# Optimization experiments

Hardware: AMD Instinct MI355X
Metric: run time of the kernel (lower is better)

## Reference

```python
import jax, jax.numpy as jnp
import numpy as np

B, D, E, G, P, H = 8192, 2048, 8, 4, 512, 192
T, DT, TAU, VTH, VRESET = 20, 0.001, 0.02, 0.5, 0.0
DELTA0, KTOP, KROUTE, PREDW = 7.0, 32, 2, 0.1


def setup_inputs() -> dict:
    key = jax.random.key(0)
    ks = jax.random.split(key, 12)
    s = 0.02
    return {
        "query_embedding": jax.random.normal(ks[0], (B, D), jnp.float32),
        "Wg": jax.random.normal(ks[1], (2, E), jnp.float32) * s,
        "bg": jnp.zeros((E,), jnp.float32),
        "Wp": jax.random.normal(ks[2], (2, E), jnp.float32) * s,
        "bp": jnp.zeros((E,), jnp.float32),
        "Wgg": jax.random.normal(ks[3], (2, G), jnp.float32) * s,
        "bgg": jnp.zeros((G,), jnp.float32),
        "W1": jax.random.normal(ks[4], (E, D, P), jnp.float32) * (1.0 / np.sqrt(D)),
        "b1": jnp.zeros((E, P), jnp.float32),
        "W2": jax.random.normal(ks[5], (E, P, D), jnp.float32) * (1.0 / np.sqrt(P)),
        "b2": jnp.zeros((E, D), jnp.float32),
    }


def reference(query_embedding, Wg, bg, Wp, bp, Wgg, bgg, W1, b1, W2, b2):
    x = query_embedding  # [B, D], already embed_dim -> no pad/slice
    dtype = x.dtype

    # --- Phasor bank temporal features on per-row mean ---
    qm = jnp.mean(x, axis=-1)  # [B]
    freqs = DELTA0 * jnp.arange(1, H + 1, dtype=dtype)  # [H]
    ang = qm[:, None] * freqs[None, :]  # [B, H]
    temporal = jnp.concatenate([jnp.cos(ang), jnp.sin(ang)], axis=-1)  # [B, 2H]

    # --- Spiking attention over top-K |x| indices (LIF over T steps) ---
    topk_idx = jax.lax.top_k(jnp.abs(x), KTOP)[1]  # [B, K]
    rows = jnp.arange(B)[:, None]
    I = jnp.zeros((B, D), dtype).at[rows, topk_idx].add(1.0)  # input current [B, vocab=D]

    def lif_step(v, _):
        v = v * (1.0 - DT / TAU) + I
        spike = (v >= VTH).astype(dtype)
        v = jnp.where(spike > 0, VRESET, v)
        return v, spike

    _, spikes = jax.lax.scan(lif_step, jnp.zeros((B, D), dtype), None, length=T)
    attention_gains = jnp.mean(spikes, axis=0)  # [B, D] spike rates

    # --- Bio gating inputs ---
    gate_in = jnp.stack([jnp.mean(temporal, axis=-1), jnp.mean(attention_gains, axis=-1)], axis=-1)  # [B, 2]

    gate_logits = gate_in @ Wg + bg  # [B, E]
    gate_logits = gate_logits - PREDW * (gate_in @ Wp + bp)

    # group routing bias: experts grouped round-robin i % G
    group_logits = gate_in @ Wgg + bgg  # [B, G]
    gmap = jax.nn.one_hot(jnp.arange(E) % G, G, dtype=dtype)  # [E, G]
    gate_logits = gate_logits + group_logits @ gmap.T

    gate_weights = jax.nn.softmax(gate_logits, axis=-1)  # temperature = 1

    # top-k routing + renormalization
    _, tidx = jax.lax.top_k(gate_weights, KROUTE)
    mask = jnp.zeros_like(gate_weights).at[rows, tidx].set(1.0)
    gated = gate_weights * mask
    gate_weights = gated / (jnp.sum(gated, axis=-1, keepdims=True) + 1e-9)

    # --- Dense MLP experts (bottleneck P = hidden // 4) ---
    h = jax.nn.relu(jnp.einsum('bd,edp->ebp', x, W1) + b1[:, None, :])  # [E, B, P]
    expert_out = jnp.einsum('ebp,eph->ebh', h, W2) + b2[:, None, :]  # [E, B, D]

    # gate-weighted combine
    context = jnp.einsum('be,ebh->bh', gate_weights, expert_out)  # [B, D]
    return context
```

## Files before the change

kernel.cpp:

```cpp
#include <hip/hip_runtime.h>
#include <stdint.h>

#define NB 8192
#define ND 2048
#define NE 8
#define NG 4
#define NP 512
#define NH 192

typedef _Float16 half_t;
typedef half_t f16x8 __attribute__((ext_vector_type(8)));
typedef float f32x4 __attribute__((ext_vector_type(4)));

__device__ __forceinline__ void gload16(const void* g, void* l) {
  __builtin_amdgcn_global_load_lds(
      (const __attribute__((address_space(1))) void*)g,
      (__attribute__((address_space(3))) void*)l, 16, 0, 0);
}

__global__ __launch_bounds__(256) void k_convert(
    const float* __restrict__ x, half_t* __restrict__ xh, double* __restrict__ qm)
{
  const int b = blockIdx.x;
  const int t = threadIdx.x;
  const float* xr = x + (size_t)b * ND;
  const float4 v0 = ((const float4*)xr)[t * 2];
  const float4 v1 = ((const float4*)xr)[t * 2 + 1];
  float f[8] = {v0.x, v0.y, v0.z, v0.w, v1.x, v1.y, v1.z, v1.w};
  double s = 0.0;
  __align__(16) half_t hb[8];
#pragma unroll
  for (int i = 0; i < 8; i++) { s += (double)f[i]; hb[i] = (half_t)f[i]; }
  *reinterpret_cast<int4*>(xh + (size_t)b * ND + t * 8) = *reinterpret_cast<const int4*>(hb);

#pragma unroll
  for (int m = 32; m >= 1; m >>= 1) s += __shfl_xor(s, m);
  __shared__ double part[4];
  if ((t & 63) == 0) part[t >> 6] = s;
  __syncthreads();
  if (t == 0) qm[b] = (part[0] + part[1] + part[2] + part[3]) / (double)ND;
}

__global__ __launch_bounds__(256) void k_gate(
    const double* __restrict__ qm,
    const float* __restrict__ Wg, const float* __restrict__ bg,
    const float* __restrict__ Wp, const float* __restrict__ bp,
    const float* __restrict__ Wgg, const float* __restrict__ bgg,
    int* __restrict__ e0a, int* __restrict__ e1a,
    float* __restrict__ w0a, float* __restrict__ w1a)
{
  const int wave = threadIdx.x >> 6;
  const int lane = threadIdx.x & 63;
  const int b = blockIdx.x * 4 + wave;
  const double q = qm[b];

  double part = 0.0;
#pragma unroll
  for (int i = 0; i < 3; i++) {
    int h = lane + i * 64;
    double ang = q * (7.0 * (double)(h + 1));
    part += cos(ang) + sin(ang);
  }
#pragma unroll
  for (int m = 32; m >= 1; m >>= 1) part += __shfl_xor(part, m);
  const double tm = part / (2.0 * (double)NH);
  const double gi1 = 32.0 / 2048.0;

  double lg = -1.0e300;
  if (lane < 8) {
    const int e = lane, g = e & 3;
    lg = tm * (double)Wg[e] + gi1 * (double)Wg[NE + e] + (double)bg[e];
    lg -= 0.1 * (tm * (double)Wp[e] + gi1 * (double)Wp[NE + e] + (double)bp[e]);
    lg += tm * (double)Wgg[g] + gi1 * (double)Wgg[NG + g] + (double)bgg[g];
  }
  double mx = lg;
#pragma unroll
  for (int m = 4; m >= 1; m >>= 1) mx = fmax(mx, __shfl_xor(mx, m));
  double pe = 0.0;
  if (lane < 8) pe = exp(lg - mx);
  double ps = pe;
#pragma unroll
  for (int m = 4; m >= 1; m >>= 1) ps += __shfl_xor(ps, m);

  double lgs[8], pes[8];
#pragma unroll
  for (int e = 0; e < 8; e++) { lgs[e] = __shfl(lg, e); pes[e] = __shfl(pe, e); }

  if (lane == 0) {
    int e0 = 0;
    for (int e = 1; e < NE; e++) if (lgs[e] > lgs[e0]) e0 = e;
    int e1 = (e0 == 0) ? 1 : 0;
    for (int e = 0; e < NE; e++) if (e != e0 && lgs[e] > lgs[e1]) e1 = e;
    const double p0 = pes[e0] / ps;
    const double p1 = pes[e1] / ps;
    const double den = p0 + p1 + 1e-9;
    e0a[b] = e0; e1a[b] = e1;
    w0a[b] = (float)(p0 / den);
    w1a[b] = (float)(p1 / den);
  }
}

__global__ __launch_bounds__(256) void k_bucket(
    const int* __restrict__ e0a, const int* __restrict__ e1a,
    const float* __restrict__ w0a, const float* __restrict__ w1a,
    int* __restrict__ rowl, float* __restrict__ wl, int* __restrict__ cnt,
    int* __restrict__ pos0a, int* __restrict__ pos1a,
    int* __restrict__ rowlp, int* __restrict__ cntp)
{
  const int t = threadIdx.x;
  const int r = blockIdx.x * 256 + t;
  __shared__ int hist[16], base[16], cursor[16];
  __shared__ int histp[64], basep[64], cursorp[64];
  if (t < 16) { hist[t] = 0; cursor[t] = 0; }
  if (t < 64) { histp[t] = 0; cursorp[t] = 0; }
  __syncthreads();

  const int e0 = e0a[r], e1 = e1a[r];
  const int p = e0 * 8 + e1;
  atomicAdd(&hist[e0], 1);
  atomicAdd(&hist[8 + e1], 1);
  atomicAdd(&histp[p], 1);
  __syncthreads();
  if (t < 16) base[t] = atomicAdd(&cnt[t], hist[t]);
  if (t < 64) basep[t] = atomicAdd(&cntp[t], histp[t]);
  __syncthreads();

  int p0 = atomicAdd(&cursor[e0], 1);
  int idx0 = base[e0] + p0;
  rowl[e0 * NB + idx0] = r;
  wl[e0 * NB + idx0] = w0a[r];
  pos0a[r] = idx0;

  int p1 = atomicAdd(&cursor[8 + e1], 1);
  int idx1 = base[8 + e1] + p1;
  rowl[(8 + e1) * NB + idx1] = r;
  wl[(8 + e1) * NB + idx1] = w1a[r];
  pos1a[r] = idx1;

  int pp = atomicAdd(&cursorp[p], 1);
  rowlp[p * NB + basep[p] + pp] = r;
}

__global__ __launch_bounds__(256) void k_cvt_w(
    const float* __restrict__ W1, const float* __restrict__ W2,
    half_t* __restrict__ w1t, half_t* __restrict__ w2t)
{
  const int which = blockIdx.y;
  const int R = which ? NP : ND;
  const int C = which ? ND : NP;
  const float* src = which ? W2 : W1;
  half_t* dst = which ? w2t : w1t;
  const int tiles_c = C >> 5;
  const int tiles_per_e = (R >> 5) * tiles_c;
  int id = blockIdx.x;
  int e = id / tiles_per_e;
  int rem = id - e * tiles_per_e;
  int tr = rem / tiles_c, tc = rem - tr * tiles_c;
  __shared__ float tile[32][33];
  const int tx = threadIdx.x & 31, ty = threadIdx.x >> 5;
  const float* s = src + (size_t)e * R * C + (size_t)(tr * 32) * C + tc * 32;
#pragma unroll
  for (int i = 0; i < 4; i++)
    tile[ty + i * 8][tx] = s[(size_t)(ty + i * 8) * C + tx];
  __syncthreads();
  half_t* d = dst + (size_t)e * R * C + (size_t)(tc * 32) * R + tr * 32;
#pragma unroll
  for (int i = 0; i < 4; i++)
    d[(size_t)(ty + i * 8) * R + tx] = (half_t)tile[tx][ty + i * 8];
}

__global__ void k_prefix(const int* __restrict__ cnt, const int* __restrict__ cntp,
                         int* __restrict__ pbase,
                         int* __restrict__ i16b, int* __restrict__ i16m, int* __restrict__ n16,
                         int* __restrict__ ipp, int* __restrict__ ipm, int* __restrict__ np)
{
  if (threadIdx.x == 0 && blockIdx.x == 0) {
    int s = 0;
    for (int i = 0; i < 16; i++) { pbase[i] = s; s += cnt[i]; }
    int t = 0;
    for (int b = 0; b < 16; b++)
      for (int m0 = 0; m0 < cnt[b]; m0 += 128) { i16b[t] = b; i16m[t] = m0; t++; }
    *n16 = t;
    t = 0;
    for (int p = 0; p < 64; p++)
      for (int m0 = 0; m0 < cntp[p]; m0 += 128) { ipp[t] = p; ipm[t] = m0; t++; }
    *np = t;
  }
}

__global__ __launch_bounds__(256, 2) void k_gemm1(
    const half_t* __restrict__ xh, const half_t* __restrict__ w1t,
    const float* __restrict__ b1,
    const int* __restrict__ rowl, const float* __restrict__ wl,
    const int* __restrict__ cnt, const int* __restrict__ pbase,
    const int* __restrict__ i16b, const int* __restrict__ i16m,
    const int* __restrict__ n16, half_t* __restrict__ Hbuf)
{
  const int wi = blockIdx.y;
  if (wi >= *n16) return;
  const int bucket = i16b[wi];
  const int m0 = i16m[wi];
  const int count = cnt[bucket];
  const int e = bucket & 7;
  const int n0 = blockIdx.x * 256;
  const int t = threadIdx.x;

  __shared__ __align__(16) half_t As[3][128 * 32];
  __shared__ __align__(16) half_t Bs[3][256 * 32];
  __shared__ int rows_s[128];
  __shared__ float ws_s[128];

  if (t < 128) {
    int mi = m0 + t;
    int idx = bucket * NB + (mi < count ? mi : m0);
    rows_s[t] = rowl[idx];
    ws_s[t] = wl[idx];
  }
  __syncthreads();

  const int w = t >> 6, lane = t & 63;
  const int cA0 = (w * 2) * 64 + lane, cA1 = cA0 + 64;
  const int rA0 = cA0 >> 2, rA1 = cA1 >> 2;
  const int kA0 = ((cA0 & 3) ^ ((rA0 >> 1) & 3)) * 8;
  const int kA1 = ((cA1 & 3) ^ ((rA1 >> 1) & 3)) * 8;
  const half_t* gA0 = xh + (size_t)rows_s[rA0] * ND + kA0;
  const half_t* gA1 = xh + (size_t)rows_s[rA1] * ND + kA1;
  const half_t* w1te = w1t + (size_t)e * NP * ND;
  const int cB0 = (w * 4) * 64 + lane, cB1 = cB0 + 64, cB2 = cB0 + 128, cB3 = cB0 + 192;
  const int rB0 = cB0 >> 2, rB1 = cB1 >> 2, rB2 = cB2 >> 2, rB3 = cB3 >> 2;
  const half_t* gB0 = w1te + (size_t)(n0 + rB0) * ND + ((cB0 & 3) ^ ((rB0 >> 1) & 3)) * 8;
  const half_t* gB1 = w1te + (size_t)(n0 + rB1) * ND + ((cB1 & 3) ^ ((rB1 >> 1) & 3)) * 8;
  const half_t* gB2 = w1te + (size_t)(n0 + rB2) * ND + ((cB2 & 3) ^ ((rB2 >> 1) & 3)) * 8;
  const half_t* gB3 = w1te + (size_t)(n0 + rB3) * ND + ((cB3 & 3) ^ ((rB3 >> 1) & 3)) * 8;

  const int wr = w >> 1, wc = w & 1;
  const int lrow = lane & 15, lk = lane >> 4;
  const int lko = (lk ^ ((lrow >> 1) & 3)) * 8;

  f32x4 acc[4][8];
#pragma unroll
  for (int i = 0; i < 4; i++)
#pragma unroll
    for (int j = 0; j < 8; j++) {
      acc[i][j][0] = 0.f; acc[i][j][1] = 0.f; acc[i][j][2] = 0.f; acc[i][j][3] = 0.f;
    }

  auto stage = [&](int bi, int tt) {
    const int kk = tt * 32;
    half_t* la = &As[bi][w * 1024];
    gload16(gA0 + kk, la);
    gload16(gA1 + kk, la + 512);
    half_t* lb = &Bs[bi][w * 2048];
    gload16(gB0 + kk, lb);
    gload16(gB1 + kk, lb + 512);
    gload16(gB2 + kk, lb + 1024);
    gload16(gB3 + kk, lb + 1536);
  };
  auto compute = [&](int bi) {
    f16x8 af[4], bf[8];
#pragma unroll
    for (int i = 0; i < 4; i++)
      af[i] = *reinterpret_cast<const f16x8*>(&As[bi][(wr * 64 + i * 16 + lrow) * 32 + lko]);
#pragma unroll
    for (int n = 0; n < 8; n++)
      bf[n] = *reinterpret_cast<const f16x8*>(&Bs[bi][(wc * 128 + n * 16 + lrow) * 32 + lko]);
#pragma unroll
    for (int mi = 0; mi < 4; mi++)
#pragma unroll
      for (int ni = 0; ni < 8; ni++)
        acc[mi][ni] = __builtin_amdgcn_mfma_f32_16x16x32_f16(af[mi], bf[ni], acc[mi][ni], 0, 0, 0);
  };

  stage(0, 0);
  stage(1, 1);
  asm volatile("s_waitcnt vmcnt(6)" ::: "memory");
  __builtin_amdgcn_s_barrier();
  for (int t3 = 0; t3 < 60; t3 += 3) {
    stage(2, t3 + 2); compute(0);
    asm volatile("s_waitcnt vmcnt(6) lgkmcnt(0)" ::: "memory");
    __builtin_amdgcn_s_barrier();
    stage(0, t3 + 3); compute(1);
    asm volatile("s_waitcnt vmcnt(6) lgkmcnt(0)" ::: "memory");
    __builtin_amdgcn_s_barrier();
    stage(1, t3 + 4); compute(2);
    asm volatile("s_waitcnt vmcnt(6) lgkmcnt(0)" ::: "memory");
    __builtin_amdgcn_s_barrier();
  }
  stage(2, 62); compute(0);
  asm volatile("s_waitcnt vmcnt(6) lgkmcnt(0)" ::: "memory");
  __builtin_amdgcn_s_barrier();
  stage(0, 63); compute(1);
  asm volatile("s_waitcnt vmcnt(6) lgkmcnt(0)" ::: "memory");
  __builtin_amdgcn_s_barrier();
  compute(2);
  asm volatile("s_waitcnt vmcnt(0) lgkmcnt(0)" ::: "memory");
  __builtin_amdgcn_s_barrier();
  compute(0);

  const int pb = pbase[bucket];
#pragma unroll
  for (int mi = 0; mi < 4; mi++) {
#pragma unroll
    for (int i = 0; i < 4; i++) {
      int lm = wr * 64 + mi * 16 + lk * 4 + i;
      if (m0 + lm < count) {
        size_t prow = (size_t)(pb + m0 + lm) * NP;
        float wcoef = ws_s[lm];
#pragma unroll
        for (int ni = 0; ni < 8; ni++) {
          int col = n0 + wc * 128 + ni * 16 + lrow;
          float v = acc[mi][ni][i] + b1[e * NP + col];
          v = v > 0.f ? v : 0.f;
          Hbuf[prow + col] = (half_t)(v * wcoef);
        }
      }
    }
  }
}

__global__ __launch_bounds__(256, 2) void k_gemm2p(
    const half_t* __restrict__ Hbuf, const half_t* __restrict__ w2t,
    const float* __restrict__ b2,
    const int* __restrict__ rowlp, const int* __restrict__ cntp,
    const int* __restrict__ pbase,
    const int* __restrict__ pos0a, const int* __restrict__ pos1a,
    const float* __restrict__ w0a, const float* __restrict__ w1a,
    const int* __restrict__ ipp, const int* __restrict__ ipm,
    const int* __restrict__ np, float* __restrict__ out)
{
  const int wi = blockIdx.y;
  if (wi >= *np) return;
  const int p = ipp[wi];
  const int m0 = ipm[wi];
  const int count = cntp[p];
  const int e0 = p >> 3, e1 = p & 7;
  const int n0 = blockIdx.x * 256;
  const int t = threadIdx.x;

  __shared__ __align__(16) half_t As[3][128 * 32];
  __shared__ __align__(16) half_t Bs[3][256 * 32];
  __shared__ int h0_s[128], h1_s[128], rs_s[128];
  __shared__ float w0_s[128], w1_s[128];

  if (t < 128) {
    int mi = m0 + t;
    int r = rowlp[p * NB + (mi < count ? mi : m0)];
    rs_s[t] = r;
    h0_s[t] = pbase[e0] + pos0a[r];
    h1_s[t] = pbase[8 + e1] + pos1a[r];
    w0_s[t] = w0a[r];
    w1_s[t] = w1a[r];
  }
  __syncthreads();

  const int w = t >> 6, lane = t & 63;
  const int cA0 = (w * 2) * 64 + lane, cA1 = cA0 + 64;
  const int rA0 = cA0 >> 2, rA1 = cA1 >> 2;
  const int kA0 = ((cA0 & 3) ^ ((rA0 >> 1) & 3)) * 8;
  const int kA1 = ((cA1 & 3) ^ ((rA1 >> 1) & 3)) * 8;
  const half_t* sa00 = Hbuf + (size_t)h0_s[rA0] * NP + kA0;
  const half_t* sa01 = Hbuf + (size_t)h0_s[rA1] * NP + kA1;
  const half_t* sa10 = Hbuf + (size_t)h1_s[rA0] * NP + kA0;
  const half_t* sa11 = Hbuf + (size_t)h1_s[rA1] * NP + kA1;

  const half_t* w2e0 = w2t + (size_t)e0 * ND * NP;
  const half_t* w2e1 = w2t + (size_t)e1 * ND * NP;
  const int cB0 = (w * 4) * 64 + lane, cB1 = cB0 + 64, cB2 = cB0 + 128, cB3 = cB0 + 192;
  const int rB0 = cB0 >> 2, rB1 = cB1 >> 2, rB2 = cB2 >> 2, rB3 = cB3 >> 2;
  const int kB0 = ((cB0 & 3) ^ ((rB0 >> 1) & 3)) * 8;
  const int kB1 = ((cB1 & 3) ^ ((rB1 >> 1) & 3)) * 8;
  const int kB2 = ((cB2 & 3) ^ ((rB2 >> 1) & 3)) * 8;
  const int kB3 = ((cB3 & 3) ^ ((rB3 >> 1) & 3)) * 8;
  const half_t* pB00 = w2e0 + (size_t)(n0 + rB0) * NP + kB0;
  const half_t* pB01 = w2e0 + (size_t)(n0 + rB1) * NP + kB1;
  const half_t* pB02 = w2e0 + (size_t)(n0 + rB2) * NP + kB2;
  const half_t* pB03 = w2e0 + (size_t)(n0 + rB3) * NP + kB3;
  const half_t* pB10 = w2e1 + (size_t)(n0 + rB0) * NP + kB0;
  const half_t* pB11 = w2e1 + (size_t)(n0 + rB1) * NP + kB1;
  const half_t* pB12 = w2e1 + (size_t)(n0 + rB2) * NP + kB2;
  const half_t* pB13 = w2e1 + (size_t)(n0 + rB3) * NP + kB3;

  const int wr = w >> 1, wc = w & 1;
  const int lrow = lane & 15, lk = lane >> 4;
  const int lko = (lk ^ ((lrow >> 1) & 3)) * 8;

  f32x4 acc[4][8];
#pragma unroll
  for (int i = 0; i < 4; i++)
#pragma unroll
    for (int j = 0; j < 8; j++) {
      acc[i][j][0] = 0.f; acc[i][j][1] = 0.f; acc[i][j][2] = 0.f; acc[i][j][3] = 0.f;
    }

  const int NT = 32;

  auto stage = [&](int bi, int tt) {
    const int kk = (tt & 15) * 32;
    half_t* la = &As[bi][w * 1024];
    half_t* lb = &Bs[bi][w * 2048];
    if (tt & 16) {
      gload16(sa10 + kk, la);
      gload16(sa11 + kk, la + 512);
      gload16(pB10 + kk, lb);
      gload16(pB11 + kk, lb + 512);
      gload16(pB12 + kk, lb + 1024);
      gload16(pB13 + kk, lb + 1536);
    } else {
      gload16(sa00 + kk, la);
      gload16(sa01 + kk, la + 512);
      gload16(pB00 + kk, lb);
      gload16(pB01 + kk, lb + 512);
      gload16(pB02 + kk, lb + 1024);
      gload16(pB03 + kk, lb + 1536);
    }
  };
  auto compute = [&](int bi) {
    f16x8 af[4], bf[8];
#pragma unroll
    for (int i = 0; i < 4; i++)
      af[i] = *reinterpret_cast<const f16x8*>(&As[bi][(wr * 64 + i * 16 + lrow) * 32 + lko]);
#pragma unroll
    for (int n = 0; n < 8; n++)
      bf[n] = *reinterpret_cast<const f16x8*>(&Bs[bi][(wc * 128 + n * 16 + lrow) * 32 + lko]);
#pragma unroll
    for (int mi = 0; mi < 4; mi++)
#pragma unroll
      for (int ni = 0; ni < 8; ni++)
        acc[mi][ni] = __builtin_amdgcn_mfma_f32_16x16x32_f16(af[mi], bf[ni], acc[mi][ni], 0, 0, 0);
  };

  stage(0, 0);
  stage(1, 1);
  asm volatile("s_waitcnt vmcnt(6)" ::: "memory");
  __builtin_amdgcn_s_barrier();
#pragma unroll
  for (int tt = 0; tt < NT; ++tt) {
    if (tt + 2 < NT) stage((tt + 2) % 3, tt + 2);
    compute(tt % 3);
    if (tt + 1 < NT) {
      if (tt + 2 < NT) asm volatile("s_waitcnt vmcnt(6) lgkmcnt(0)" ::: "memory");
      else             asm volatile("s_waitcnt vmcnt(0) lgkmcnt(0)" ::: "memory");
      __builtin_amdgcn_s_barrier();
    }
  }

  float b20[8], b21[8];
#pragma unroll
  for (int ni = 0; ni < 8; ni++) {
    int col = n0 + wc * 128 + ni * 16 + lrow;
    b20[ni] = b2[e0 * ND + col];
    b21[ni] = b2[e1 * ND + col];
  }
#pragma unroll
  for (int mi = 0; mi < 4; mi++) {
#pragma unroll
    for (int i = 0; i < 4; i++) {
      int lm = wr * 64 + mi * 16 + lk * 4 + i;
      if (m0 + lm < count) {
        int r = rs_s[lm];
        float wb0 = w0_s[lm], wb1 = w1_s[lm];
        float* orow = out + (size_t)r * ND;
#pragma unroll
        for (int ni = 0; ni < 8; ni++) {
          int col = n0 + wc * 128 + ni * 16 + lrow;
          orow[col] = acc[mi][ni][i] + wb0 * b20[ni] + wb1 * b21[ni];
        }
      }
    }
  }
}

extern "C" void kernel_launch(void* const* d_in, const int* in_sizes, int n_in,
                              void* d_out, int out_size, void* d_ws, size_t ws_size,
                              hipStream_t stream)
{
  const float* x   = (const float*)d_in[0];
  const float* Wg  = (const float*)d_in[1];
  const float* bg  = (const float*)d_in[2];
  const float* Wp  = (const float*)d_in[3];
  const float* bp  = (const float*)d_in[4];
  const float* Wgg = (const float*)d_in[5];
  const float* bgg = (const float*)d_in[6];
  const float* W1  = (const float*)d_in[7];
  const float* b1  = (const float*)d_in[8];
  const float* W2  = (const float*)d_in[9];
  const float* b2  = (const float*)d_in[10];
  float* out = (float*)d_out;

  char* ws = (char*)d_ws;
  size_t off = 0;
  const size_t OFF_XH   = off; off += (size_t)NB * ND * 2;
  const size_t OFF_W1T  = off; off += (size_t)NE * NP * ND * 2;
  const size_t OFF_W2T  = off; off += (size_t)NE * ND * NP * 2;
  const size_t OFF_H    = off; off += (size_t)(2 * NB + 128) * NP * 2;
  const size_t OFF_ROWL = off; off += (size_t)16 * NB * 4;
  const size_t OFF_WL   = off; off += (size_t)16 * NB * 4;
  const size_t OFF_ROWLP= off; off += (size_t)64 * NB * 4;
  const size_t OFF_CNT  = off; off += 64;
  const size_t OFF_CNTP = off; off += 256;
  const size_t OFF_PB   = off; off += 64;
  const size_t OFF_QM   = off; off += (size_t)NB * 8;
  const size_t OFF_E0   = off; off += (size_t)NB * 4;
  const size_t OFF_E1   = off; off += (size_t)NB * 4;
  const size_t OFF_W0   = off; off += (size_t)NB * 4;
  const size_t OFF_W1A  = off; off += (size_t)NB * 4;
  const size_t OFF_POS0 = off; off += (size_t)NB * 4;
  const size_t OFF_POS1 = off; off += (size_t)NB * 4;
  const size_t OFF_I16B = off; off += 1024;
  const size_t OFF_I16M = off; off += 1024;
  const size_t OFF_N16  = off; off += 64;
  const size_t OFF_IPP  = off; off += 1024;
  const size_t OFF_IPM  = off; off += 1024;
  const size_t OFF_NP   = off; off += 64;

  half_t* xh   = (half_t*)(ws + OFF_XH);
  half_t* w1t  = (half_t*)(ws + OFF_W1T);
  half_t* w2t  = (half_t*)(ws + OFF_W2T);
  half_t* Hbuf = (half_t*)(ws + OFF_H);
  int*    rowl = (int*)(ws + OFF_ROWL);
  float*  wl   = (float*)(ws + OFF_WL);
  int*    rowlp= (int*)(ws + OFF_ROWLP);
  int*    cnt  = (int*)(ws + OFF_CNT);
  int*    cntp = (int*)(ws + OFF_CNTP);
  int*    pb   = (int*)(ws + OFF_PB);
  double* qm   = (double*)(ws + OFF_QM);
  int*    e0a  = (int*)(ws + OFF_E0);
  int*    e1a  = (int*)(ws + OFF_E1);
  float*  w0a  = (float*)(ws + OFF_W0);
  float*  w1a  = (float*)(ws + OFF_W1A);
  int*    pos0a= (int*)(ws + OFF_POS0);
  int*    pos1a= (int*)(ws + OFF_POS1);
  int*    i16b = (int*)(ws + OFF_I16B);
  int*    i16m = (int*)(ws + OFF_I16M);
  int*    n16  = (int*)(ws + OFF_N16);
  int*    ipp  = (int*)(ws + OFF_IPP);
  int*    ipm  = (int*)(ws + OFF_IPM);
  int*    np   = (int*)(ws + OFF_NP);

  hipMemsetAsync(cnt, 0, 64 + 256, stream);
  k_convert<<<NB, 256, 0, stream>>>(x, xh, qm);
  k_cvt_w<<<dim3(8192, 2, 1), 256, 0, stream>>>(W1, W2, w1t, w2t);
  k_gate<<<NB / 4, 256, 0, stream>>>(qm, Wg, bg, Wp, bp, Wgg, bgg, e0a, e1a, w0a, w1a);
  k_bucket<<<NB / 256, 256, 0, stream>>>(e0a, e1a, w0a, w1a, rowl, wl, cnt,
                                         pos0a, pos1a, rowlp, cntp);
  k_prefix<<<1, 64, 0, stream>>>(cnt, cntp, pb, i16b, i16m, n16, ipp, ipm, np);
  k_gemm1<<<dim3(2, 144, 1), 256, 0, stream>>>(xh, w1t, b1, rowl, wl, cnt, pb,
                                               i16b, i16m, n16, Hbuf);
  k_gemm2p<<<dim3(8, 128, 1), 256, 0, stream>>>(Hbuf, w2t, b2, rowlp, cntp, pb,
                                                 pos0a, pos1a, w0a, w1a, ipp, ipm, np, out);
}
```

Baseline: 360.7 us.

## Shrink gemm2 N-tile to 128, vectorize weight transpose stores, split prefix scans

```diff
diff --git a/kernel.cpp b/kernel.cpp
--- a/kernel.cpp
+++ b/kernel.cpp
@@ -151,22 +151,27 @@
   const float* src = which ? W2 : W1;
   half_t* dst = which ? w2t : w1t;
   const int tiles_c = C >> 5;
-  const int tiles_per_e = (R >> 5) * tiles_c;
+  const int tiles_per_e = (R >> 6) * tiles_c;
   int id = blockIdx.x;
   int e = id / tiles_per_e;
   int rem = id - e * tiles_per_e;
   int tr = rem / tiles_c, tc = rem - tr * tiles_c;
-  __shared__ float tile[32][33];
-  const int tx = threadIdx.x & 31, ty = threadIdx.x >> 5;
-  const float* s = src + (size_t)e * R * C + (size_t)(tr * 32) * C + tc * 32;
-#pragma unroll
-  for (int i = 0; i < 4; i++)
-    tile[ty + i * 8][tx] = s[(size_t)(ty + i * 8) * C + tx];
-  __syncthreads();
-  half_t* d = dst + (size_t)e * R * C + (size_t)(tc * 32) * R + tr * 32;
-#pragma unroll
-  for (int i = 0; i < 4; i++)
-    d[(size_t)(ty + i * 8) * R + tx] = (half_t)tile[tx][ty + i * 8];
+  __shared__ float tile[64][33];
+  const int t = threadIdx.x;
+
+  const int lc = t & 31, lr = t >> 5;
+  const float* s = src + (size_t)e * R * C + (size_t)(tr * 64) * C + tc * 32;
+#pragma unroll
+  for (int i = 0; i < 8; i++)
+    tile[lr + i * 8][lc] = s[(size_t)(lr + i * 8) * C + lc];
+  __syncthreads();
+
+  const int n = t >> 3, kc = (t & 7) * 8;
+  __align__(16) half_t hb[8];
+#pragma unroll
+  for (int j = 0; j < 8; j++) hb[j] = (half_t)tile[kc + j][n];
+  half_t* d = dst + (size_t)e * R * C + (size_t)(tc * 32 + n) * R + tr * 64 + kc;
+  *reinterpret_cast<int4*>(d) = *reinterpret_cast<const int4*>(hb);
 }
 
 __global__ void k_prefix(const int* __restrict__ cnt, const int* __restrict__ cntp,
@@ -174,17 +179,26 @@
                          int* __restrict__ i16b, int* __restrict__ i16m, int* __restrict__ n16,
                          int* __restrict__ ipp, int* __restrict__ ipm, int* __restrict__ np)
 {
-  if (threadIdx.x == 0 && blockIdx.x == 0) {
+  const int t = threadIdx.x;
+  if (t == 0) {
+    int c[16];
+#pragma unroll
+    for (int i = 0; i < 16; i++) c[i] = cnt[i];
     int s = 0;
-    for (int i = 0; i < 16; i++) { pbase[i] = s; s += cnt[i]; }
-    int t = 0;
+#pragma unroll
+    for (int i = 0; i < 16; i++) { pbase[i] = s; s += c[i]; }
+    int k = 0;
     for (int b = 0; b < 16; b++)
-      for (int m0 = 0; m0 < cnt[b]; m0 += 128) { i16b[t] = b; i16m[t] = m0; t++; }
-    *n16 = t;
-    t = 0;
+      for (int m0 = 0; m0 < c[b]; m0 += 128) { i16b[k] = b; i16m[k] = m0; k++; }
+    *n16 = k;
+  } else if (t == 64) {
+    int c[64];
+#pragma unroll
+    for (int i = 0; i < 64; i++) c[i] = cntp[i];
+    int k = 0;
     for (int p = 0; p < 64; p++)
-      for (int m0 = 0; m0 < cntp[p]; m0 += 128) { ipp[t] = p; ipm[t] = m0; t++; }
-    *np = t;
+      for (int m0 = 0; m0 < c[p]; m0 += 128) { ipp[k] = p; ipm[k] = m0; k++; }
+    *np = k;
   }
 }
 
@@ -318,7 +332,7 @@
   }
 }
 
-__global__ __launch_bounds__(256, 2) void k_gemm2p(
+__global__ __launch_bounds__(256) void k_gemm2p(
     const half_t* __restrict__ Hbuf, const half_t* __restrict__ w2t,
     const float* __restrict__ b2,
     const int* __restrict__ rowlp, const int* __restrict__ cntp,
@@ -334,11 +348,11 @@
   const int m0 = ipm[wi];
   const int count = cntp[p];
   const int e0 = p >> 3, e1 = p & 7;
-  const int n0 = blockIdx.x * 256;
+  const int n0 = blockIdx.x * 128;
   const int t = threadIdx.x;
 
   __shared__ __align__(16) half_t As[3][128 * 32];
-  __shared__ __align__(16) half_t Bs[3][256 * 32];
+  __shared__ __align__(16) half_t Bs[3][128 * 32];
   __shared__ int h0_s[128], h1_s[128], rs_s[128];
   __shared__ float w0_s[128], w1_s[128];
 
@@ -354,41 +368,30 @@
   __syncthreads();
 
   const int w = t >> 6, lane = t & 63;
-  const int cA0 = (w * 2) * 64 + lane, cA1 = cA0 + 64;
-  const int rA0 = cA0 >> 2, rA1 = cA1 >> 2;
-  const int kA0 = ((cA0 & 3) ^ ((rA0 >> 1) & 3)) * 8;
-  const int kA1 = ((cA1 & 3) ^ ((rA1 >> 1) & 3)) * 8;
-  const half_t* sa00 = Hbuf + (size_t)h0_s[rA0] * NP + kA0;
-  const half_t* sa01 = Hbuf + (size_t)h0_s[rA1] * NP + kA1;
-  const half_t* sa10 = Hbuf + (size_t)h1_s[rA0] * NP + kA0;
-  const half_t* sa11 = Hbuf + (size_t)h1_s[rA1] * NP + kA1;
-
+  const int c0 = w * 128 + lane, c1 = c0 + 64;
+  const int row0 = c0 >> 2, ch0 = c0 & 3;
+  const int row1 = c1 >> 2, ch1 = c1 & 3;
+  const int sw0 = (row0 >> 1) & 3, sw1 = (row1 >> 1) & 3;
   const half_t* w2e0 = w2t + (size_t)e0 * ND * NP;
   const half_t* w2e1 = w2t + (size_t)e1 * ND * NP;
-  const int cB0 = (w * 4) * 64 + lane, cB1 = cB0 + 64, cB2 = cB0 + 128, cB3 = cB0 + 192;
-  const int rB0 = cB0 >> 2, rB1 = cB1 >> 2, rB2 = cB2 >> 2, rB3 = cB3 >> 2;
-  const int kB0 = ((cB0 & 3) ^ ((rB0 >> 1) & 3)) * 8;
-  const int kB1 = ((cB1 & 3) ^ ((rB1 >> 1) & 3)) * 8;
-  const int kB2 = ((cB2 & 3) ^ ((rB2 >> 1) & 3)) * 8;
-  const int kB3 = ((cB3 & 3) ^ ((rB3 >> 1) & 3)) * 8;
-  const half_t* pB00 = w2e0 + (size_t)(n0 + rB0) * NP + kB0;
-  const half_t* pB01 = w2e0 + (size_t)(n0 + rB1) * NP + kB1;
-  const half_t* pB02 = w2e0 + (size_t)(n0 + rB2) * NP + kB2;
-  const half_t* pB03 = w2e0 + (size_t)(n0 + rB3) * NP + kB3;
-  const half_t* pB10 = w2e1 + (size_t)(n0 + rB0) * NP + kB0;
-  const half_t* pB11 = w2e1 + (size_t)(n0 + rB1) * NP + kB1;
-  const half_t* pB12 = w2e1 + (size_t)(n0 + rB2) * NP + kB2;
-  const half_t* pB13 = w2e1 + (size_t)(n0 + rB3) * NP + kB3;
+  const half_t* sa00 = Hbuf + (size_t)h0_s[row0] * NP + ((ch0 ^ sw0) * 8);
+  const half_t* sa01 = Hbuf + (size_t)h0_s[row1] * NP + ((ch1 ^ sw1) * 8);
+  const half_t* sa10 = Hbuf + (size_t)h1_s[row0] * NP + ((ch0 ^ sw0) * 8);
+  const half_t* sa11 = Hbuf + (size_t)h1_s[row1] * NP + ((ch1 ^ sw1) * 8);
+  const half_t* pB00 = w2e0 + (size_t)(n0 + row0) * NP + ((ch0 ^ sw0) * 8);
+  const half_t* pB01 = w2e0 + (size_t)(n0 + row1) * NP + ((ch1 ^ sw1) * 8);
+  const half_t* pB10 = w2e1 + (size_t)(n0 + row0) * NP + ((ch0 ^ sw0) * 8);
+  const half_t* pB11 = w2e1 + (size_t)(n0 + row1) * NP + ((ch1 ^ sw1) * 8);
 
   const int wr = w >> 1, wc = w & 1;
   const int lrow = lane & 15, lk = lane >> 4;
   const int lko = (lk ^ ((lrow >> 1) & 3)) * 8;
 
-  f32x4 acc[4][8];
+  f32x4 acc[4][4];
 #pragma unroll
   for (int i = 0; i < 4; i++)
 #pragma unroll
-    for (int j = 0; j < 8; j++) {
+    for (int j = 0; j < 4; j++) {
       acc[i][j][0] = 0.f; acc[i][j][1] = 0.f; acc[i][j][2] = 0.f; acc[i][j][3] = 0.f;
     }
 
@@ -397,57 +400,52 @@
   auto stage = [&](int bi, int tt) {
     const int kk = (tt & 15) * 32;
     half_t* la = &As[bi][w * 1024];
-    half_t* lb = &Bs[bi][w * 2048];
+    half_t* lb = &Bs[bi][w * 1024];
     if (tt & 16) {
       gload16(sa10 + kk, la);
       gload16(sa11 + kk, la + 512);
       gload16(pB10 + kk, lb);
       gload16(pB11 + kk, lb + 512);
-      gload16(pB12 + kk, lb + 1024);
-      gload16(pB13 + kk, lb + 1536);
     } else {
       gload16(sa00 + kk, la);
       gload16(sa01 + kk, la + 512);
       gload16(pB00 + kk, lb);
       gload16(pB01 + kk, lb + 512);
-      gload16(pB02 + kk, lb + 1024);
-      gload16(pB03 + kk, lb + 1536);
     }
   };
   auto compute = [&](int bi) {
-    f16x8 af[4], bf[8];
-#pragma unroll
-    for (int i = 0; i < 4; i++)
+    f16x8 af[4], bf[4];
+#pragma unroll
+    for (int i = 0; i < 4; i++) {
       af[i] = *reinterpret_cast<const f16x8*>(&As[bi][(wr * 64 + i * 16 + lrow) * 32 + lko]);
-#pragma unroll
-    for (int n = 0; n < 8; n++)
-      bf[n] = *reinterpret_cast<const f16x8*>(&Bs[bi][(wc * 128 + n * 16 + lrow) * 32 + lko]);
+      bf[i] = *reinterpret_cast<const f16x8*>(&Bs[bi][(wc * 64 + i * 16 + lrow) * 32 + lko]);
+    }
 #pragma unroll
     for (int mi = 0; mi < 4; mi++)
 #pragma unroll
-      for (int ni = 0; ni < 8; ni++)
+      for (int ni = 0; ni < 4; ni++)
         acc[mi][ni] = __builtin_amdgcn_mfma_f32_16x16x32_f16(af[mi], bf[ni], acc[mi][ni], 0, 0, 0);
   };
 
   stage(0, 0);
   stage(1, 1);
-  asm volatile("s_waitcnt vmcnt(6)" ::: "memory");
+  asm volatile("s_waitcnt vmcnt(4)" ::: "memory");
   __builtin_amdgcn_s_barrier();
 #pragma unroll
   for (int tt = 0; tt < NT; ++tt) {
     if (tt + 2 < NT) stage((tt + 2) % 3, tt + 2);
     compute(tt % 3);
     if (tt + 1 < NT) {
-      if (tt + 2 < NT) asm volatile("s_waitcnt vmcnt(6) lgkmcnt(0)" ::: "memory");
+      if (tt + 2 < NT) asm volatile("s_waitcnt vmcnt(4) lgkmcnt(0)" ::: "memory");
       else             asm volatile("s_waitcnt vmcnt(0) lgkmcnt(0)" ::: "memory");
       __builtin_amdgcn_s_barrier();
     }
   }
 
-  float b20[8], b21[8];
-#pragma unroll
-  for (int ni = 0; ni < 8; ni++) {
-    int col = n0 + wc * 128 + ni * 16 + lrow;
+  float b20[4], b21[4];
+#pragma unroll
+  for (int ni = 0; ni < 4; ni++) {
+    int col = n0 + wc * 64 + ni * 16 + lrow;
     b20[ni] = b2[e0 * ND + col];
     b21[ni] = b2[e1 * ND + col];
   }
@@ -461,8 +459,8 @@
         float wb0 = w0_s[lm], wb1 = w1_s[lm];
         float* orow = out + (size_t)r * ND;
 #pragma unroll
-        for (int ni = 0; ni < 8; ni++) {
-          int col = n0 + wc * 128 + ni * 16 + lrow;
+        for (int ni = 0; ni < 4; ni++) {
+          int col = n0 + wc * 64 + ni * 16 + lrow;
           orow[col] = acc[mi][ni][i] + wb0 * b20[ni] + wb1 * b21[ni];
         }
       }
@@ -539,13 +537,13 @@
 
   hipMemsetAsync(cnt, 0, 64 + 256, stream);
   k_convert<<<NB, 256, 0, stream>>>(x, xh, qm);
-  k_cvt_w<<<dim3(8192, 2, 1), 256, 0, stream>>>(W1, W2, w1t, w2t);
+  k_cvt_w<<<dim3(4096, 2, 1), 256, 0, stream>>>(W1, W2, w1t, w2t);
   k_gate<<<NB / 4, 256, 0, stream>>>(qm, Wg, bg, Wp, bp, Wgg, bgg, e0a, e1a, w0a, w1a);
   k_bucket<<<NB / 256, 256, 0, stream>>>(e0a, e1a, w0a, w1a, rowl, wl, cnt,
                                          pos0a, pos1a, rowlp, cntp);
-  k_prefix<<<1, 64, 0, stream>>>(cnt, cntp, pb, i16b, i16m, n16, ipp, ipm, np);
+  k_prefix<<<1, 128, 0, stream>>>(cnt, cntp, pb, i16b, i16m, n16, ipp, ipm, np);
   k_gemm1<<<dim3(2, 144, 1), 256, 0, stream>>>(xh, w1t, b1, rowl, wl, cnt, pb,
                                                i16b, i16m, n16, Hbuf);
-  k_gemm2p<<<dim3(8, 128, 1), 256, 0, stream>>>(Hbuf, w2t, b2, rowlp, cntp, pb,
+  k_gemm2p<<<dim3(16, 128, 1), 256, 0, stream>>>(Hbuf, w2t, b2, rowlp, cntp, pb,
                                                  pos0a, pos1a, w0a, w1a, ipp, ipm, np, out);
 }
```

New measurement: 343.0 us. 1.05x faster.
